# Performance work log

Measured on AMD Instinct MI355X. Metric: run time of the kernel, lower is better.

The kernel has to match this reference:

```python
import jax, jax.numpy as jnp
import numpy as np

B, N, K = 16, 4096, 128

def setup_inputs() -> dict:
    key = jax.random.key(0)
    k1, k2, k3, k4, k5 = jax.random.split(key, 5)
    positions = jax.random.normal(k1, (B, N, 3), dtype=jnp.float32) * 5.0
    neighbors = jax.random.randint(k2, (B, N, K), 0, N, dtype=jnp.int32)
    neighbor_mask = (jax.random.uniform(k3, (B, N, K)) < 0.9).astype(jnp.float32)
    cell = jax.random.normal(k4, (B, 3, 3), dtype=jnp.float32) + 10.0 * jnp.eye(3, dtype=jnp.float32)
    cell_offsets = jax.random.randint(k5, (B, N, K, 3), -1, 2).astype(jnp.float32)
    return {
        "positions": positions,
        "neighbors": neighbors,
        "neighbor_mask": neighbor_mask,
        "cell": cell,
        "cell_offsets": cell_offsets,
    }

def reference(positions, neighbors, neighbor_mask, cell, cell_offsets):
    # Gather neighbor positions: [B,N,K,3]
    pos_j = jax.vmap(lambda p, n: p[n])(positions, neighbors)
    # Relative vectors r_j - r_i
    dist_vec = pos_j - positions[:, :, None, :]
    # Periodic boundary correction: offsets @ cell, [B,N,K,3]
    dist_vec = dist_vec + jnp.einsum("bnkd,bde->bnke", cell_offsets, cell)
    sq = jnp.sum(dist_vec * dist_vec, axis=-1)  # [B,N,K]
    mask = neighbor_mask > 0
    # Masked distances (safe sqrt: avoid sqrt(0) grad issues on masked entries)
    distances = jnp.where(mask, jnp.sqrt(jnp.where(mask, sq, 1.0)), 0.0)
    return distances
```

## Files before the change

kernel.cpp:

```cpp
#include <hip/hip_runtime.h>
#include <math.h>

constexpr int B = 16;
constexpr int N = 4096;
constexpr int K = 128;

__global__ __launch_bounds__(256)
void pairwise_dist_kernel(const float* __restrict__ pos,
                          const int*   __restrict__ nbr,
                          const float* __restrict__ mask,
                          const float* __restrict__ cell,
                          const float* __restrict__ offs,
                          float*       __restrict__ out) {
    const int t = blockIdx.x * blockDim.x + threadIdx.x;
    const long long e0 = (long long)t * 4;
    if (e0 >= (long long)B * N * K) return;

    const int row = (int)(e0 >> 7);
    const int b   = row >> 12;
    const int n   = row & (N - 1);

    const float* __restrict__ pb = pos + (size_t)b * N * 3;
    const float xi = pb[n * 3 + 0];
    const float yi = pb[n * 3 + 1];
    const float zi = pb[n * 3 + 2];

    const float* __restrict__ cb = cell + b * 9;
    const float c00 = cb[0], c01 = cb[1], c02 = cb[2];
    const float c10 = cb[3], c11 = cb[4], c12 = cb[5];
    const float c20 = cb[6], c21 = cb[7], c22 = cb[8];

    const int4   jj = *(const int4*)  (nbr  + e0);
    const float4 mm = *(const float4*)(mask + e0);
    const float4 o0 = *(const float4*)(offs + e0 * 3);
    const float4 o1 = *(const float4*)(offs + e0 * 3 + 4);
    const float4 o2 = *(const float4*)(offs + e0 * 3 + 8);

    const float ox[4] = {o0.x, o0.w, o1.z, o2.y};
    const float oy[4] = {o0.y, o1.x, o1.w, o2.z};
    const float oz[4] = {o0.z, o1.y, o2.x, o2.w};
    const int   j [4] = {jj.x, jj.y, jj.z, jj.w};
    const float m [4] = {mm.x, mm.y, mm.z, mm.w};

    float res[4];
#pragma unroll
    for (int i = 0; i < 4; ++i) {
        const float* __restrict__ pj = pb + (size_t)j[i] * 3;
        const float dx = (pj[0] - xi) + ox[i] * c00 + oy[i] * c10 + oz[i] * c20;
        const float dy = (pj[1] - yi) + ox[i] * c01 + oy[i] * c11 + oz[i] * c21;
        const float dz = (pj[2] - zi) + ox[i] * c02 + oy[i] * c12 + oz[i] * c22;
        const float sq = dx * dx + dy * dy + dz * dz;
        res[i] = (m[i] > 0.0f) ? sqrtf(sq) : 0.0f;
    }

    *(float4*)(out + e0) = make_float4(res[0], res[1], res[2], res[3]);
}

extern "C" void kernel_launch(void* const* d_in, const int* in_sizes, int n_in,
                              void* d_out, int out_size, void* d_ws, size_t ws_size,
                              hipStream_t stream) {
    const float* positions     = (const float*)d_in[0];
    const int*   neighbors     = (const int*)  d_in[1];
    const float* neighbor_mask = (const float*)d_in[2];
    const float* cell          = (const float*)d_in[3];
    const float* cell_offsets  = (const float*)d_in[4];
    float*       out           = (float*)d_out;

    const long long total   = (long long)B * N * K;
    const int       threads = 256;
    const long long nthread = total / 4;
    const int       blocks  = (int)((nthread + threads - 1) / threads);

    pairwise_dist_kernel<<<blocks, threads, 0, stream>>>(
        positions, neighbors, neighbor_mask, cell, cell_offsets, out);
}
```

Before: 225.7 us.

## Stage per-batch positions in LDS and gather neighbors from shared memory

Each 1024-thread block loads the whole batch's position array (4096 points) into shared memory as padded float4, then handles 64 rows with two iterations per thread, gathering neighbor positions from LDS rather than global memory. This removes scattered global gathers, which were likely served from L2. In exchange each block re-reads 48KB of positions and uses 64KB of LDS, which limits occupancy and adds a block-wide barrier.

```diff
diff --git a/kernel.cpp b/kernel.cpp
--- a/kernel.cpp
+++ b/kernel.cpp
@@ -5,55 +5,78 @@
 constexpr int N = 4096;
 constexpr int K = 128;
 
-__global__ __launch_bounds__(256)
-void pairwise_dist_kernel(const float* __restrict__ pos,
-                          const int*   __restrict__ nbr,
-                          const float* __restrict__ mask,
-                          const float* __restrict__ cell,
-                          const float* __restrict__ offs,
-                          float*       __restrict__ out) {
-    const int t = blockIdx.x * blockDim.x + threadIdx.x;
-    const long long e0 = (long long)t * 4;
-    if (e0 >= (long long)B * N * K) return;
+constexpr int ROWS_PER_BLOCK = 64;
+constexpr int THREADS = 1024;
 
-    const int row = (int)(e0 >> 7);
-    const int b   = row >> 12;
-    const int n   = row & (N - 1);
+__global__ __launch_bounds__(THREADS)
+void pairwise_dist_lds(const float* __restrict__ pos,
+                       const int*   __restrict__ nbr,
+                       const float* __restrict__ mask,
+                       const float* __restrict__ cell,
+                       const float* __restrict__ offs,
+                       float*       __restrict__ out) {
+    __shared__ float4 spos[N];
 
-    const float* __restrict__ pb = pos + (size_t)b * N * 3;
-    const float xi = pb[n * 3 + 0];
-    const float yi = pb[n * 3 + 1];
-    const float zi = pb[n * 3 + 2];
+    const int tid   = threadIdx.x;
+    const int b     = blockIdx.x >> 6;
+    const int rblk  = blockIdx.x & 63;
+    const int nbase = rblk * ROWS_PER_BLOCK;
+
+    {
+        const float4* __restrict__ pb4 =
+            (const float4*)(pos + (size_t)b * N * 3);
+        const float4 r0 = pb4[tid * 3 + 0];
+        const float4 r1 = pb4[tid * 3 + 1];
+        const float4 r2 = pb4[tid * 3 + 2];
+        const int a0 = tid * 4;
+        spos[a0 + 0] = make_float4(r0.x, r0.y, r0.z, 0.f);
+        spos[a0 + 1] = make_float4(r0.w, r1.x, r1.y, 0.f);
+        spos[a0 + 2] = make_float4(r1.z, r1.w, r2.x, 0.f);
+        spos[a0 + 3] = make_float4(r2.y, r2.z, r2.w, 0.f);
+    }
 
     const float* __restrict__ cb = cell + b * 9;
     const float c00 = cb[0], c01 = cb[1], c02 = cb[2];
     const float c10 = cb[3], c11 = cb[4], c12 = cb[5];
     const float c20 = cb[6], c21 = cb[7], c22 = cb[8];
 
-    const int4   jj = *(const int4*)  (nbr  + e0);
-    const float4 mm = *(const float4*)(mask + e0);
-    const float4 o0 = *(const float4*)(offs + e0 * 3);
-    const float4 o1 = *(const float4*)(offs + e0 * 3 + 4);
-    const float4 o2 = *(const float4*)(offs + e0 * 3 + 8);
+    __syncthreads();
 
-    const float ox[4] = {o0.x, o0.w, o1.z, o2.y};
-    const float oy[4] = {o0.y, o1.x, o1.w, o2.z};
-    const float oz[4] = {o0.z, o1.y, o2.x, o2.w};
-    const int   j [4] = {jj.x, jj.y, jj.z, jj.w};
-    const float m [4] = {mm.x, mm.y, mm.z, mm.w};
+    const size_t blockElemBase = ((size_t)b * N + nbase) * K;
 
-    float res[4];
 #pragma unroll
-    for (int i = 0; i < 4; ++i) {
-        const float* __restrict__ pj = pb + (size_t)j[i] * 3;
-        const float dx = (pj[0] - xi) + ox[i] * c00 + oy[i] * c10 + oz[i] * c20;
-        const float dy = (pj[1] - yi) + ox[i] * c01 + oy[i] * c11 + oz[i] * c21;
-        const float dz = (pj[2] - zi) + ox[i] * c02 + oy[i] * c12 + oz[i] * c22;
-        const float sq = dx * dx + dy * dy + dz * dz;
-        res[i] = (m[i] > 0.0f) ? sqrtf(sq) : 0.0f;
+    for (int it = 0; it < 2; ++it) {
+        const int    eLocal = it * 4096 + tid * 4;
+        const size_t e0     = blockElemBase + eLocal;
+        const int    n      = nbase + (eLocal >> 7);
+
+        const float4 pi = spos[n];
+
+        const int4   jj = *(const int4*)  (nbr  + e0);
+        const float4 mm = *(const float4*)(mask + e0);
+        const float4 o0 = *(const float4*)(offs + e0 * 3);
+        const float4 o1 = *(const float4*)(offs + e0 * 3 + 4);
+        const float4 o2 = *(const float4*)(offs + e0 * 3 + 8);
+
+        const float ox[4] = {o0.x, o0.w, o1.z, o2.y};
+        const float oy[4] = {o0.y, o1.x, o1.w, o2.z};
+        const float oz[4] = {o0.z, o1.y, o2.x, o2.w};
+        const int   j [4] = {jj.x, jj.y, jj.z, jj.w};
+        const float m [4] = {mm.x, mm.y, mm.z, mm.w};
+
+        float res[4];
+#pragma unroll
+        for (int i = 0; i < 4; ++i) {
+            const float4 pj = spos[j[i]];
+            const float dx = (pj.x - pi.x) + ox[i] * c00 + oy[i] * c10 + oz[i] * c20;
+            const float dy = (pj.y - pi.y) + ox[i] * c01 + oy[i] * c11 + oz[i] * c21;
+            const float dz = (pj.z - pi.z) + ox[i] * c02 + oy[i] * c12 + oz[i] * c22;
+            const float sq = dx * dx + dy * dy + dz * dz;
+            res[i] = (m[i] > 0.0f) ? sqrtf(sq) : 0.0f;
+        }
+
+        *(float4*)(out + e0) = make_float4(res[0], res[1], res[2], res[3]);
     }
-
-    *(float4*)(out + e0) = make_float4(res[0], res[1], res[2], res[3]);
 }
 
 extern "C" void kernel_launch(void* const* d_in, const int* in_sizes, int n_in,
@@ -66,11 +89,8 @@
     const float* cell_offsets  = (const float*)d_in[4];
     float*       out           = (float*)d_out;
 
-    const long long total   = (long long)B * N * K;
-    const int       threads = 256;
-    const long long nthread = total / 4;
-    const int       blocks  = (int)((nthread + threads - 1) / threads);
+    const int blocks = B * (N / ROWS_PER_BLOCK);
 
-    pairwise_dist_kernel<<<blocks, threads, 0, stream>>>(
+    pairwise_dist_lds<<<blocks, THREADS, 0, stream>>>(
         positions, neighbors, neighbor_mask, cell, cell_offsets, out);
 }
```

Result: faster. 214.5 us (-5.0%).

## Pack positions to float4 for single-load gathers and use nontemporal streaming

Applied to the files above, without the earlier changes.

Adds a pre-pass that repacks positions into 16-byte padded float4 entries in workspace, so each neighbor gather becomes one vector load instead of three scalar loads. Streaming inputs and output use nontemporal load/store hints to keep the gathered position table resident in cache, and sqrt uses the raw hardware builtin. It costs an extra kernel launch and workspace usage, and falls back to unpacked loads if workspace is too small.

```diff
diff --git a/kernel.cpp b/kernel.cpp
--- a/kernel.cpp
+++ b/kernel.cpp
@@ -5,36 +5,54 @@
 constexpr int N = 4096;
 constexpr int K = 128;
 
+typedef float fx4 __attribute__((ext_vector_type(4)));
+typedef int   ix4 __attribute__((ext_vector_type(4)));
+
 __global__ __launch_bounds__(256)
-void pairwise_dist_kernel(const float* __restrict__ pos,
-                          const int*   __restrict__ nbr,
-                          const float* __restrict__ mask,
-                          const float* __restrict__ cell,
-                          const float* __restrict__ offs,
-                          float*       __restrict__ out) {
-    const int t = blockIdx.x * blockDim.x + threadIdx.x;
-    const long long e0 = (long long)t * 4;
-    if (e0 >= (long long)B * N * K) return;
+void pack_positions(const float* __restrict__ pos, fx4* __restrict__ packed) {
+    const int t = blockIdx.x * 256 + threadIdx.x;
+    const fx4* __restrict__ p4 = (const fx4*)pos;
+    const fx4 r0 = p4[t * 3 + 0];
+    const fx4 r1 = p4[t * 3 + 1];
+    const fx4 r2 = p4[t * 3 + 2];
+    packed[t * 4 + 0] = (fx4){r0.x, r0.y, r0.z, 0.f};
+    packed[t * 4 + 1] = (fx4){r0.w, r1.x, r1.y, 0.f};
+    packed[t * 4 + 2] = (fx4){r1.z, r1.w, r2.x, 0.f};
+    packed[t * 4 + 3] = (fx4){r2.y, r2.z, r2.w, 0.f};
+}
 
-    const int row = (int)(e0 >> 7);
-    const int b   = row >> 12;
-    const int n   = row & (N - 1);
+template <bool PACKED>
+__global__ __launch_bounds__(256, 8)
+void pairwise_dist_g(const fx4*   __restrict__ packed,
+                     const float* __restrict__ pos,
+                     const int*   __restrict__ nbr,
+                     const float* __restrict__ mask,
+                     const float* __restrict__ cell,
+                     const float* __restrict__ offs,
+                     float*       __restrict__ out) {
+    const int    t   = blockIdx.x * 256 + threadIdx.x;
+    const size_t e0  = (size_t)t * 4;
+    const int    row = (int)(e0 >> 7);
+    const int    b   = row >> 12;
 
-    const float* __restrict__ pb = pos + (size_t)b * N * 3;
-    const float xi = pb[n * 3 + 0];
-    const float yi = pb[n * 3 + 1];
-    const float zi = pb[n * 3 + 2];
+    const ix4 jj = __builtin_nontemporal_load((const ix4*)(nbr  + e0));
+    const fx4 mm = __builtin_nontemporal_load((const fx4*)(mask + e0));
+    const fx4 o0 = __builtin_nontemporal_load((const fx4*)(offs + e0 * 3));
+    const fx4 o1 = __builtin_nontemporal_load((const fx4*)(offs + e0 * 3 + 4));
+    const fx4 o2 = __builtin_nontemporal_load((const fx4*)(offs + e0 * 3 + 8));
+
+    fx4 pi;
+    if (PACKED) {
+        pi = packed[row];
+    } else {
+        const float* __restrict__ p = pos + (size_t)row * 3;
+        pi = (fx4){p[0], p[1], p[2], 0.f};
+    }
 
     const float* __restrict__ cb = cell + b * 9;
     const float c00 = cb[0], c01 = cb[1], c02 = cb[2];
     const float c10 = cb[3], c11 = cb[4], c12 = cb[5];
     const float c20 = cb[6], c21 = cb[7], c22 = cb[8];
-
-    const int4   jj = *(const int4*)  (nbr  + e0);
-    const float4 mm = *(const float4*)(mask + e0);
-    const float4 o0 = *(const float4*)(offs + e0 * 3);
-    const float4 o1 = *(const float4*)(offs + e0 * 3 + 4);
-    const float4 o2 = *(const float4*)(offs + e0 * 3 + 8);
 
     const float ox[4] = {o0.x, o0.w, o1.z, o2.y};
     const float oy[4] = {o0.y, o1.x, o1.w, o2.z};
@@ -45,15 +63,22 @@
     float res[4];
 #pragma unroll
     for (int i = 0; i < 4; ++i) {
-        const float* __restrict__ pj = pb + (size_t)j[i] * 3;
-        const float dx = (pj[0] - xi) + ox[i] * c00 + oy[i] * c10 + oz[i] * c20;
-        const float dy = (pj[1] - yi) + ox[i] * c01 + oy[i] * c11 + oz[i] * c21;
-        const float dz = (pj[2] - zi) + ox[i] * c02 + oy[i] * c12 + oz[i] * c22;
+        fx4 pj;
+        if (PACKED) {
+            pj = packed[(b << 12) + j[i]];
+        } else {
+            const float* __restrict__ p = pos + ((size_t)(b << 12) + j[i]) * 3;
+            pj = (fx4){p[0], p[1], p[2], 0.f};
+        }
+        const float dx = (pj.x - pi.x) + ox[i] * c00 + oy[i] * c10 + oz[i] * c20;
+        const float dy = (pj.y - pi.y) + ox[i] * c01 + oy[i] * c11 + oz[i] * c21;
+        const float dz = (pj.z - pi.z) + ox[i] * c02 + oy[i] * c12 + oz[i] * c22;
         const float sq = dx * dx + dy * dy + dz * dz;
-        res[i] = (m[i] > 0.0f) ? sqrtf(sq) : 0.0f;
+        res[i] = (m[i] > 0.0f) ? __builtin_amdgcn_sqrtf(sq) : 0.0f;
     }
 
-    *(float4*)(out + e0) = make_float4(res[0], res[1], res[2], res[3]);
+    const fx4 r = {res[0], res[1], res[2], res[3]};
+    __builtin_nontemporal_store(r, (fx4*)(out + e0));
 }
 
 extern "C" void kernel_launch(void* const* d_in, const int* in_sizes, int n_in,
@@ -66,11 +91,16 @@
     const float* cell_offsets  = (const float*)d_in[4];
     float*       out           = (float*)d_out;
 
-    const long long total   = (long long)B * N * K;
-    const int       threads = 256;
-    const long long nthread = total / 4;
-    const int       blocks  = (int)((nthread + threads - 1) / threads);
+    const size_t packedBytes = (size_t)B * N * sizeof(fx4);
+    const int    mainBlocks  = (B * N * K) / (256 * 4);
 
-    pairwise_dist_kernel<<<blocks, threads, 0, stream>>>(
-        positions, neighbors, neighbor_mask, cell, cell_offsets, out);
+    if (ws_size >= packedBytes) {
+        fx4* packed = (fx4*)d_ws;
+        pack_positions<<<(B * N / 4) / 256, 256, 0, stream>>>(positions, packed);
+        pairwise_dist_g<true><<<mainBlocks, 256, 0, stream>>>(
+            packed, positions, neighbors, neighbor_mask, cell, cell_offsets, out);
+    } else {
+        pairwise_dist_g<false><<<mainBlocks, 256, 0, stream>>>(
+            nullptr, positions, neighbors, neighbor_mask, cell, cell_offsets, out);
+    }
 }
```

New measurement: 232.1 us. +2.8%, slower.
